# Performance work log

Hardware: AMD Instinct MI355X
Metric: run time of the kernel (lower is better)

Reference implementation:

```python
import jax, jax.numpy as jnp
import numpy as np

V, E, H = 32000, 512, 1024
B, T = 32, 48
PAD = 0


def setup_inputs() -> dict:
    key = jax.random.key(0)
    ks = jax.random.split(key, 9)
    s = 0.05
    emb = jax.random.normal(ks[0], (V, E), jnp.float32) * s
    emb = emb.at[PAD].set(0.0)  # padding_idx row is zero in nn.Embedding
    return {
        "initial_hidden_state": jax.random.normal(ks[1], (B, H), jnp.float32),
        "target_sequence": jax.random.randint(ks[2], (B, T), 0, V),
        "emb": emb,
        "W_ih": jax.random.normal(ks[3], (3 * H, E), jnp.float32) * s,  # [r;z;n] input weights
        "W_hh": jax.random.normal(ks[4], (3 * H, H), jnp.float32) * s,
        "b_ih": jax.random.normal(ks[5], (3 * H,), jnp.float32) * s,
        "b_hh": jax.random.normal(ks[6], (3 * H,), jnp.float32) * s,
        "W_cls": jax.random.normal(ks[7], (V, H), jnp.float32) * s,
        "b_cls": jax.random.normal(ks[8], (V,), jnp.float32) * s,
    }


def _decode(initial_hidden_state, target_sequence, emb, W_ih, W_hh, b_ih, b_hh, W_cls, b_cls):
    # teacher forcing: sample_probability = 0.0 -> use_sample False
    idx_t = target_sequence.T  # [T, B]

    def step(h, y_idx):
        x = emb[y_idx]                                 # [B, E] embedding gather
        gi = x @ W_ih.T + b_ih                         # [B, 3H]
        gh = h @ W_hh.T + b_hh                         # [B, 3H]
        i_r, i_z, i_n = jnp.split(gi, 3, axis=-1)
        h_r, h_z, h_n = jnp.split(gh, 3, axis=-1)
        r = jax.nn.sigmoid(i_r + h_r)
        z = jax.nn.sigmoid(i_z + h_z)
        n = jnp.tanh(i_n + r * h_n)
        h_new = (1.0 - z) * n + z * h                  # torch GRUCell update
        score = h_new @ W_cls.T + b_cls                # [B, V]
        return h_new, score

    _, scores = jax.lax.scan(step, initial_hidden_state, idx_t)  # [T, B, V]
    return jnp.transpose(scores, (1, 0, 2))                      # [B, T, V]


def reference(initial_hidden_state, target_sequence, emb, W_ih, W_hh, b_ih, b_hh, W_cls, b_cls):
    return _decode(initial_hidden_state, target_sequence, emb, W_ih, W_hh, b_ih, b_hh, W_cls, b_cls)
```

## Files before the change

### kernel.cpp

```cpp
#include <hip/hip_runtime.h>
#include <hip/hip_bf16.h>

typedef __attribute__((ext_vector_type(8))) short short8;
typedef __attribute__((ext_vector_type(4))) float f32x4;

#define T_STEPS 48
#define BATCH 32
#define EDIM 512
#define HDIM 1024
#define VOCAB 32000
#define GRU_BLOCKS 64
#define JPB 16
#define SENT 0x7FFF7FFFu
#define N_TILES 750
#define CNT_STRIDE 16
#define EARLY_WORKERS 128

#define HS_T_STRIDE 16384

__device__ __forceinline__ unsigned short f2bf(float f) {
    __hip_bfloat16 h = __float2bfloat16(f);
    return *reinterpret_cast<unsigned short*>(&h);
}
__device__ __forceinline__ float bf2f(unsigned short u) {
    union { unsigned int i; float f; } v;
    v.i = ((unsigned int)u) << 16;
    return v.f;
}

typedef __attribute__((address_space(1))) const void GAS;
typedef __attribute__((address_space(3))) void LAS;
__device__ __forceinline__ void gload_lds16(const unsigned short* g, unsigned short* l) {
    __builtin_amdgcn_global_load_lds((GAS*)g, (LAS*)(unsigned)(uintptr_t)l, 16, 0, 0);
}

__global__ __launch_bounds__(256) void prep_kernel(
    const float* __restrict__ h0, const int* __restrict__ tseq,
    const float* __restrict__ emb, const float* __restrict__ w_ih,
    const float* __restrict__ w_hh, const float* __restrict__ w_cls,
    unsigned short* __restrict__ wcls_bf, unsigned short* __restrict__ wih_bf,
    unsigned short* __restrict__ whh_bf, unsigned short* __restrict__ x_bf,
    unsigned int* __restrict__ hs32, unsigned int* __restrict__ cnt8)
{
    const long R0 = (long)VOCAB * HDIM / 4;
    const long R1 = (long)3 * HDIM * EDIM / 4;
    const long R2 = (long)3 * HDIM * HDIM / 4;
    const long R3 = (long)T_STEPS * BATCH * EDIM / 4;
    const long R4 = (long)HS_T_STRIDE;
    const long R5 = (long)T_STEPS * HS_T_STRIDE / 4;
    const long R6 = 512;
    const long total = R0 + R1 + R2 + R3 + R4 + R5 + R6;

    for (long i = (long)blockIdx.x * blockDim.x + threadIdx.x; i < total;
         i += (long)gridDim.x * blockDim.x) {
        if (i < R0) {
            float4 v = reinterpret_cast<const float4*>(w_cls)[i];
            ushort4 u = { f2bf(v.x), f2bf(v.y), f2bf(v.z), f2bf(v.w) };
            *reinterpret_cast<ushort4*>(wcls_bf + i * 4) = u;
        } else if (i < R0 + R1) {
            long j = i - R0;
            float4 v = reinterpret_cast<const float4*>(w_ih)[j];
            ushort4 u = { f2bf(v.x), f2bf(v.y), f2bf(v.z), f2bf(v.w) };
            *reinterpret_cast<ushort4*>(wih_bf + j * 4) = u;
        } else if (i < R0 + R1 + R2) {
            long j = i - R0 - R1;
            float4 v = reinterpret_cast<const float4*>(w_hh)[j];
            ushort4 u = { f2bf(v.x), f2bf(v.y), f2bf(v.z), f2bf(v.w) };
            *reinterpret_cast<ushort4*>(whh_bf + j * 4) = u;
        } else if (i < R0 + R1 + R2 + R3) {
            long j = i - R0 - R1 - R2;
            int m = (int)(j >> 7);
            int kk4 = (int)(j & 127);
            int t = m >> 5, b = m & 31;
            int tok = tseq[b * T_STEPS + t];
            float4 v = reinterpret_cast<const float4*>(emb)[(long)tok * (EDIM / 4) + kk4];
            ushort4 u = { f2bf(v.x), f2bf(v.y), f2bf(v.z), f2bf(v.w) };
            *reinterpret_cast<ushort4*>(x_bf + (long)m * EDIM + kk4 * 4) = u;
        } else if (i < R0 + R1 + R2 + R3 + R4) {
            long j = i - R0 - R1 - R2 - R3;
            int w = (int)(j >> 5), b = (int)(j & 31);
            unsigned short a = f2bf(h0[b * HDIM + 2 * w]);
            unsigned short c = f2bf(h0[b * HDIM + 2 * w + 1]);
            hs32[j] = (unsigned)a | ((unsigned)c << 16);
        } else if (i < R0 + R1 + R2 + R3 + R4 + R5) {
            long j = i - R0 - R1 - R2 - R3 - R4;
            uint4 s = { SENT, SENT, SENT, SENT };
            reinterpret_cast<uint4*>(hs32 + HS_T_STRIDE)[j] = s;
        } else {
            long j = i - R0 - R1 - R2 - R3 - R4 - R5;
            uint4 z = { 0u, 0u, 0u, 0u };
            reinterpret_cast<uint4*>(cnt8)[j] = z;
        }
    }
}

__global__ __launch_bounds__(256) void gemm_gi(
    const unsigned short* __restrict__ A, const unsigned short* __restrict__ B,
    const float* __restrict__ bias, float* __restrict__ C, int K, int Ntot, int nM)
{
    const int nwg = gridDim.x;
    const int lin = blockIdx.x;
    const int q = nwg >> 3;
    const int wg = (lin & 7) * q + (lin >> 3);
    const int mi = wg % nM, ni = wg / nM;
    const int m0 = mi * 128, n0 = ni * 128;

    const int tid = threadIdx.x;
    const int lane = tid & 63;
    const int wid = tid >> 6;
    const int wr = wid >> 1, wc = wid & 1;

    __shared__ __align__(16) unsigned short As[128 * 32];
    __shared__ __align__(16) unsigned short Bs[128 * 32];

    f32x4 acc[4][4] = {};
    const int NT = K >> 5;
    const int srow = (lane >> 2);
    const int skk = (lane & 3) * 8;

    for (int kt = 0; kt < NT; ++kt) {
        __syncthreads();
        {
            const int kb = kt * 32;
#pragma unroll
            for (int h2 = 0; h2 < 2; ++h2) {
                const int i = wid + h2 * 4;
                const int row = i * 16 + srow;
                gload_lds16(A + (size_t)(m0 + row) * K + kb + skk, As + i * 512);
                gload_lds16(B + (size_t)(n0 + row) * K + kb + skk, Bs + i * 512);
            }
        }
        __syncthreads();

        const int kg = lane >> 4;
        const int l15 = lane & 15;
        short8 af[4], bf[4];
#pragma unroll
        for (int i = 0; i < 4; ++i) {
            af[i] = *(const short8*)(As + ((wr * 64 + i * 16 + l15) * 32 + kg * 8));
            bf[i] = *(const short8*)(Bs + ((wc * 64 + i * 16 + l15) * 32 + kg * 8));
        }
#pragma unroll
        for (int i = 0; i < 4; ++i)
#pragma unroll
            for (int j = 0; j < 4; ++j)
                acc[i][j] = __builtin_amdgcn_mfma_f32_16x16x32_bf16(af[i], bf[j], acc[i][j], 0, 0, 0);
    }

    const int l15 = lane & 15, lhi = lane >> 4;
#pragma unroll
    for (int i = 0; i < 4; ++i)
#pragma unroll
        for (int j = 0; j < 4; ++j) {
            int col = n0 + wc * 64 + j * 16 + l15;
            float bv = bias[col];
#pragma unroll
            for (int q2 = 0; q2 < 4; ++q2) {
                int row = m0 + wr * 64 + i * 16 + lhi * 4 + q2;
                C[(size_t)row * Ntot + col] = acc[i][j][q2] + bv;
            }
        }
}

__global__ __launch_bounds__(512, 1) void fused_kernel(
    unsigned int* __restrict__ hs32, unsigned int* __restrict__ hrow32,
    const unsigned short* __restrict__ whh_bf,
    const float* __restrict__ gi, const float* __restrict__ b_hh,
    const float* __restrict__ h0,
    const unsigned short* __restrict__ wcls_bf, const float* __restrict__ b_cls,
    float* __restrict__ out, unsigned int* __restrict__ cnt8,
    unsigned int* __restrict__ tileq)
{
    __shared__ __align__(16) unsigned short Wl[48][1032];
    __shared__ float P[4][32][49];
    __shared__ __align__(16) unsigned short As[256 * 32];
    __shared__ __align__(16) unsigned short Bs[256 * 32];
    __shared__ int sTile;

    const int tid = threadIdx.x;
    const int bid = blockIdx.x;
    const int lane = tid & 63, wid = tid >> 6;
    const int l15 = lane & 15, kg = lane >> 4;

    if (bid < GRU_BLOCKS) {
        const int j0 = bid * JPB;
        for (int c = tid; c < 48 * 128; c += 512) {
            int row = c >> 7, k8 = (c & 127) * 8;
            int g = row >> 4, jj = row & 15;
            *(short8*)&Wl[row][k8] =
                *(const short8*)(whh_bf + (size_t)(g * HDIM + j0 + jj) * HDIM + k8);
        }
        const int b = tid >> 4, jj = tid & 15;
        const int gj = j0 + jj;
        const float bhr = b_hh[gj];
        const float bhz = b_hh[HDIM + gj];
        const float bhn = b_hh[2 * HDIM + gj];
        float hloc = h0[b * HDIM + gj];
        __syncthreads();

        for (int t = 0; t < T_STEPS; ++t) {
            const size_t tb = (size_t)t * HS_T_STRIDE;
            const float* gr = gi + (size_t)(t * BATCH + b) * (3 * HDIM);
            float xr = gr[gj], xz = gr[HDIM + gj], xn = gr[2 * HDIM + gj];

            if (t) {
                if (wid == 0) {
                    const unsigned int* cp = cnt8 + (size_t)t * CNT_STRIDE;
                    for (;;) {
                        unsigned v = (lane < 8)
                            ? __hip_atomic_load(cp + lane, __ATOMIC_RELAXED, __HIP_MEMORY_SCOPE_AGENT)
                            : 8u;
                        if (__all(v >= 8u)) break;
                        __builtin_amdgcn_s_sleep(2);
                    }
                }
                __syncthreads();
                asm volatile("" ::: "memory");
            }

            if (tid < 256) {
                const int kq = wid * 256;
                unsigned wv[8][8];
#pragma unroll
                for (int ks = 0; ks < 8; ++ks) {
                    const int wbase = wid * 128 + ks * 16 + kg * 4;
#pragma unroll
                    for (int mi2 = 0; mi2 < 2; ++mi2) {
                        const int bb = mi2 * 16 + l15;
#pragma unroll
                        for (int q = 0; q < 4; ++q)
                            wv[ks][mi2 * 4 + q] = *(const unsigned*)(
                                hs32 + tb + (size_t)(wbase + q) * 32 + bb);
                    }
                }
                for (;;) {
                    int bad = 0;
#pragma unroll
                    for (int ks = 0; ks < 8; ++ks)
#pragma unroll
                        for (int i = 0; i < 8; ++i)
                            bad |= (wv[ks][i] == SENT);
                    if (!__any(bad)) break;
                    __builtin_amdgcn_s_sleep(1);
#pragma unroll
                    for (int ks = 0; ks < 8; ++ks)
#pragma unroll
                        for (int i = 0; i < 8; ++i)
                            if (wv[ks][i] == SENT) {
                                const int mi2 = i >> 2, q = i & 3;
                                wv[ks][i] = __hip_atomic_load(
                                    hs32 + tb + (size_t)(wid * 128 + ks * 16 + kg * 4 + q) * 32 + (mi2 * 16 + l15),
                                    __ATOMIC_RELAXED, __HIP_MEMORY_SCOPE_AGENT);
                            }
                }
                f32x4 acc[2][3] = {};
#pragma unroll
                for (int ks = 0; ks < 8; ++ks) {
                    const int kb = kq + ks * 32 + kg * 8;
                    union U8 { unsigned u[4]; short8 s; };
                    short8 ah[2];
#pragma unroll
                    for (int mi2 = 0; mi2 < 2; ++mi2) {
                        U8 x;
#pragma unroll
                        for (int q = 0; q < 4; ++q) x.u[q] = wv[ks][mi2 * 4 + q];
                        ah[mi2] = x.s;
                    }
#pragma unroll
                    for (int fr = 0; fr < 3; ++fr) {
                        short8 bh = *(const short8*)&Wl[fr * 16 + l15][kb];
#pragma unroll
                        for (int mi2 = 0; mi2 < 2; ++mi2)
                            acc[mi2][fr] = __builtin_amdgcn_mfma_f32_16x16x32_bf16(ah[mi2], bh, acc[mi2][fr], 0, 0, 0);
                    }
                }
#pragma unroll
                for (int mi2 = 0; mi2 < 2; ++mi2)
#pragma unroll
                    for (int fr = 0; fr < 3; ++fr)
#pragma unroll
                        for (int q = 0; q < 4; ++q)
                            P[wid][mi2 * 16 + kg * 4 + q][fr * 16 + l15] = acc[mi2][fr][q];
            }
            __syncthreads();

            {
                float ghr = 0.f, ghz = 0.f, ghn = 0.f;
#pragma unroll
                for (int w = 0; w < 4; ++w) {
                    ghr += P[w][b][jj];
                    ghz += P[w][b][16 + jj];
                    ghn += P[w][b][32 + jj];
                }
                float r = 1.f / (1.f + __expf(-(xr + ghr + bhr)));
                float z = 1.f / (1.f + __expf(-(xz + ghz + bhz)));
                float n = tanhf(xn + r * (ghn + bhn));
                float hnew = (1.f - z) * n + z * hloc;
                hloc = hnew;
                unsigned hv = f2bf(hnew);
                unsigned nb = (unsigned)__shfl_xor((int)hv, 1);
                if (!(jj & 1)) {
                    unsigned w1 = hv | (nb << 16);
                    const int wdx = gj >> 1;
                    __hip_atomic_store(hs32 + (size_t)(t + 1) * HS_T_STRIDE + (size_t)wdx * 32 + b,
                                       w1, __ATOMIC_RELAXED, __HIP_MEMORY_SCOPE_AGENT);
                    __hip_atomic_store(hrow32 + ((size_t)t * BATCH + b) * 512 + wdx,
                                       w1, __ATOMIC_RELAXED, __HIP_MEMORY_SCOPE_AGENT);
                }
            }
            __syncthreads();
            if (tid == 0)
                __hip_atomic_fetch_add(cnt8 + (size_t)(t + 1) * CNT_STRIDE + (bid & 7), 1u,
                                       __ATOMIC_RELAXED, __HIP_MEMORY_SCOPE_AGENT);
        }
    } else if (bid >= GRU_BLOCKS + EARLY_WORKERS) {
        if (wid == 0) {
            const unsigned int* cp = cnt8 + (size_t)T_STEPS * CNT_STRIDE;
            for (;;) {
                unsigned v = (lane < 8)
                    ? __hip_atomic_load(cp + lane, __ATOMIC_RELAXED, __HIP_MEMORY_SCOPE_AGENT)
                    : 8u;
                if (__all(v >= 8u)) break;
                __builtin_amdgcn_s_sleep(64);
            }
        }
        __syncthreads();
    }

    const unsigned short* hrowA = (const unsigned short*)hrow32;
    const int srow = lane >> 2;
    const int skk = (lane & 3) * 8;
    const int wm = wid >> 1, wn = wid & 1;

    for (;;) {
        __syncthreads();
        if (tid == 0)
            sTile = (int)__hip_atomic_fetch_add(tileq, 1u, __ATOMIC_RELAXED, __HIP_MEMORY_SCOPE_AGENT);
        __syncthreads();
        const int k = sTile;
        if (k >= N_TILES) break;
        const int mi = k / 125, ni = k - mi * 125;
        const int m0 = mi * 256, n0 = ni * 256;

        {
            if (wid == 0) {
                const unsigned int* cp = cnt8 + (size_t)(mi * 8 + 8) * CNT_STRIDE;
                for (;;) {
                    unsigned v = (lane < 8)
                        ? __hip_atomic_load(cp + lane, __ATOMIC_RELAXED, __HIP_MEMORY_SCOPE_AGENT)
                        : 8u;
                    if (__all(v >= 8u)) break;
                    __builtin_amdgcn_s_sleep(32);
                }
            }
            __syncthreads();
            asm volatile("" ::: "memory");
        }

        f32x4 acc[4][8] = {};
        for (int kt = 0; kt < 32; ++kt) {
            __syncthreads();
            {
                const int kb = kt * 32;
#pragma unroll
                for (int h2 = 0; h2 < 2; ++h2) {
                    const int i = wid + h2 * 8;
                    const int row = i * 16 + srow;
                    gload_lds16(hrowA + (size_t)(m0 + row) * HDIM + kb + skk, As + i * 512);
                    gload_lds16(wcls_bf + (size_t)(n0 + row) * HDIM + kb + skk, Bs + i * 512);
                }
            }
            __syncthreads();

            short8 af[4], bf[8];
#pragma unroll
            for (int i = 0; i < 4; ++i)
                af[i] = *(const short8*)(As + ((wm * 64 + i * 16 + l15) * 32 + kg * 8));
#pragma unroll
            for (int j = 0; j < 8; ++j)
                bf[j] = *(const short8*)(Bs + ((wn * 128 + j * 16 + l15) * 32 + kg * 8));
#pragma unroll
            for (int i = 0; i < 4; ++i)
#pragma unroll
                for (int j = 0; j < 8; ++j)
                    acc[i][j] = __builtin_amdgcn_mfma_f32_16x16x32_bf16(af[i], bf[j], acc[i][j], 0, 0, 0);
        }

        const int lhi = lane >> 4;
#pragma unroll
        for (int i = 0; i < 4; ++i)
#pragma unroll
            for (int j = 0; j < 8; ++j) {
                int col = n0 + wn * 128 + j * 16 + l15;
                float bv = b_cls[col];
#pragma unroll
                for (int q2 = 0; q2 < 4; ++q2) {
                    int row = m0 + wm * 64 + i * 16 + lhi * 4 + q2;
                    int t = row >> 5, bb = row & 31;
                    __builtin_nontemporal_store(acc[i][j][q2] + bv,
                        &out[(size_t)(bb * T_STEPS + t) * VOCAB + col]);
                }
            }
    }
}

extern "C" void kernel_launch(void* const* d_in, const int* in_sizes, int n_in,
                              void* d_out, int out_size, void* d_ws, size_t ws_size,
                              hipStream_t stream) {
    const float* h0    = (const float*)d_in[0];
    const int*   tseq  = (const int*)d_in[1];
    const float* emb   = (const float*)d_in[2];
    const float* w_ih  = (const float*)d_in[3];
    const float* w_hh  = (const float*)d_in[4];
    const float* b_ih  = (const float*)d_in[5];
    const float* b_hh  = (const float*)d_in[6];
    const float* w_cls = (const float*)d_in[7];
    const float* b_cls = (const float*)d_in[8];
    float* out = (float*)d_out;

    char* w = (char*)d_ws;
    unsigned short* wcls_bf = (unsigned short*)w; w += (size_t)VOCAB * HDIM * 2;
    unsigned short* wih_bf  = (unsigned short*)w; w += (size_t)3 * HDIM * EDIM * 2;
    unsigned short* whh_bf  = (unsigned short*)w; w += (size_t)3 * HDIM * HDIM * 2;
    unsigned short* x_bf    = (unsigned short*)w; w += (size_t)T_STEPS * BATCH * EDIM * 2;
    unsigned int*   hs32    = (unsigned int*)w;   w += (size_t)(T_STEPS + 1) * HS_T_STRIDE * 4;
    unsigned int*   hrow32  = (unsigned int*)w;   w += (size_t)T_STEPS * BATCH * 512 * 4;
    float* gi               = (float*)w;          w += (size_t)T_STEPS * BATCH * 3 * HDIM * 4;
    unsigned int* cnt8      = (unsigned int*)w;   w += 8192;
    unsigned int* tileq     = cnt8 + 1024;

    prep_kernel<<<2048, 256, 0, stream>>>(h0, tseq, emb, w_ih, w_hh, w_cls,
                                          wcls_bf, wih_bf, whh_bf, x_bf, hs32, cnt8);

    gemm_gi<<<(T_STEPS * BATCH / 128) * (3 * HDIM / 128), 256, 0, stream>>>(
        x_bf, wih_bf, b_ih, gi, EDIM, 3 * HDIM, T_STEPS * BATCH / 128);

    fused_kernel<<<256, 512, 0, stream>>>(hs32, hrow32, whh_bf, gi, b_hh, h0,
                                          wcls_bf, b_cls, out, cnt8, tileq);
}
```

Before: 384.0 us.

## Double-buffer classifier GEMM LDS tiles and vectorize hidden-state publication

The classifier GEMM loop now uses two LDS buffers so that the global-to-LDS load for the next K slice is issued while MFMAs run on the current one, removing one barrier per K step. Shared memory is unioned between the GRU weight cache and the GEMM buffers to make room for this. The GRU blocks also stage new hidden values in LDS and publish them with 16-byte coherent (sc0 sc1) stores instead of many scalar atomic stores. The risk is that the second buffer's loads may not be waited for correctly, and that the recurrence path gains an extra barrier per step.

```diff
diff --git a/kernel.cpp b/kernel.cpp
--- a/kernel.cpp
+++ b/kernel.cpp
@@ -3,6 +3,7 @@
 
 typedef __attribute__((ext_vector_type(8))) short short8;
 typedef __attribute__((ext_vector_type(4))) float f32x4;
+typedef __attribute__((ext_vector_type(4))) unsigned int u32x4;
 
 #define T_STEPS 48
 #define BATCH 32
@@ -32,6 +33,11 @@
 typedef __attribute__((address_space(3))) void LAS;
 __device__ __forceinline__ void gload_lds16(const unsigned short* g, unsigned short* l) {
     __builtin_amdgcn_global_load_lds((GAS*)g, (LAS*)(unsigned)(uintptr_t)l, 16, 0, 0);
+}
+
+__device__ __forceinline__ void store16_coh(unsigned int* p, u32x4 v) {
+    asm volatile("global_store_dwordx4 %0, %1, off sc0 sc1"
+                 :: "v"((unsigned long long)(uintptr_t)p), "v"(v) : "memory");
 }
 
 __global__ __launch_bounds__(256) void prep_kernel(
@@ -171,10 +177,8 @@
     float* __restrict__ out, unsigned int* __restrict__ cnt8,
     unsigned int* __restrict__ tileq)
 {
-    __shared__ __align__(16) unsigned short Wl[48][1032];
-    __shared__ float P[4][32][49];
-    __shared__ __align__(16) unsigned short As[256 * 32];
-    __shared__ __align__(16) unsigned short Bs[256 * 32];
+    __shared__ __align__(16) char smem[124160];
+    __shared__ unsigned short Hs[BATCH][JPB];
     __shared__ int sTile;
 
     const int tid = threadIdx.x;
@@ -183,6 +187,9 @@
     const int l15 = lane & 15, kg = lane >> 4;
 
     if (bid < GRU_BLOCKS) {
+        unsigned short (*Wl)[1032] = reinterpret_cast<unsigned short (*)[1032]>(smem);
+        float (*P)[32][49] = reinterpret_cast<float (*)[32][49]>(smem + 99072);
+
         const int j0 = bid * JPB;
         for (int c = tid; c < 48 * 128; c += 512) {
             int row = c >> 7, k8 = (c & 127) * 8;
@@ -297,16 +304,28 @@
                 float n = tanhf(xn + r * (ghn + bhn));
                 float hnew = (1.f - z) * n + z * hloc;
                 hloc = hnew;
-                unsigned hv = f2bf(hnew);
-                unsigned nb = (unsigned)__shfl_xor((int)hv, 1);
-                if (!(jj & 1)) {
-                    unsigned w1 = hv | (nb << 16);
-                    const int wdx = gj >> 1;
-                    __hip_atomic_store(hs32 + (size_t)(t + 1) * HS_T_STRIDE + (size_t)wdx * 32 + b,
-                                       w1, __ATOMIC_RELAXED, __HIP_MEMORY_SCOPE_AGENT);
-                    __hip_atomic_store(hrow32 + ((size_t)t * BATCH + b) * 512 + wdx,
-                                       w1, __ATOMIC_RELAXED, __HIP_MEMORY_SCOPE_AGENT);
-                }
+                Hs[b][jj] = f2bf(hnew);
+            }
+            __syncthreads();
+
+            if (tid < 64) {
+                const int q = tid >> 3, c = tid & 7;
+                u32x4 d;
+#pragma unroll
+                for (int w2 = 0; w2 < 4; ++w2) {
+                    int bb = c * 4 + w2;
+                    d[w2] = (unsigned)Hs[bb][2 * q] | ((unsigned)Hs[bb][2 * q + 1] << 16);
+                }
+                store16_coh(hs32 + (size_t)(t + 1) * HS_T_STRIDE + (size_t)((j0 >> 1) + q) * 32 + c * 4, d);
+            } else if (tid < 128) {
+                const int i = tid - 64, bb = i >> 1, half = i & 1;
+                u32x4 d;
+#pragma unroll
+                for (int w2 = 0; w2 < 4; ++w2) {
+                    int q = half * 4 + w2;
+                    d[w2] = (unsigned)Hs[bb][2 * q] | ((unsigned)Hs[bb][2 * q + 1] << 16);
+                }
+                store16_coh(hrow32 + ((size_t)t * BATCH + bb) * 512 + (j0 >> 1) + half * 4, d);
             }
             __syncthreads();
             if (tid == 0)
@@ -332,6 +351,11 @@
     const int skk = (lane & 3) * 8;
     const int wm = wid >> 1, wn = wid & 1;
 
+    unsigned short* As0 = (unsigned short*)(smem);
+    unsigned short* Bs0 = (unsigned short*)(smem + 16384);
+    unsigned short* As1 = (unsigned short*)(smem + 32768);
+    unsigned short* Bs1 = (unsigned short*)(smem + 49152);
+
     for (;;) {
         __syncthreads();
         if (tid == 0)
@@ -358,33 +382,47 @@
         }
 
         f32x4 acc[4][8] = {};
-        for (int kt = 0; kt < 32; ++kt) {
-            __syncthreads();
-            {
-                const int kb = kt * 32;
-#pragma unroll
-                for (int h2 = 0; h2 < 2; ++h2) {
-                    const int i = wid + h2 * 8;
-                    const int row = i * 16 + srow;
-                    gload_lds16(hrowA + (size_t)(m0 + row) * HDIM + kb + skk, As + i * 512);
-                    gload_lds16(wcls_bf + (size_t)(n0 + row) * HDIM + kb + skk, Bs + i * 512);
-                }
-            }
-            __syncthreads();
-
-            short8 af[4], bf[8];
-#pragma unroll
-            for (int i = 0; i < 4; ++i)
-                af[i] = *(const short8*)(As + ((wm * 64 + i * 16 + l15) * 32 + kg * 8));
-#pragma unroll
-            for (int j = 0; j < 8; ++j)
-                bf[j] = *(const short8*)(Bs + ((wn * 128 + j * 16 + l15) * 32 + kg * 8));
-#pragma unroll
-            for (int i = 0; i < 4; ++i)
-#pragma unroll
-                for (int j = 0; j < 8; ++j)
-                    acc[i][j] = __builtin_amdgcn_mfma_f32_16x16x32_bf16(af[i], bf[j], acc[i][j], 0, 0, 0);
-        }
+
+#define STAGE(KT, AB, BB)                                                      \
+        {                                                                      \
+            const int kb = (KT) * 32;                                          \
+            _Pragma("unroll")                                                  \
+            for (int h2 = 0; h2 < 2; ++h2) {                                   \
+                const int i = wid + h2 * 8;                                    \
+                const int row = i * 16 + srow;                                 \
+                gload_lds16(hrowA + (size_t)(m0 + row) * HDIM + kb + skk, (AB) + i * 512); \
+                gload_lds16(wcls_bf + (size_t)(n0 + row) * HDIM + kb + skk, (BB) + i * 512); \
+            }                                                                  \
+        }
+#define COMPUTE(AB, BB)                                                        \
+        {                                                                      \
+            short8 af[4], bf[8];                                               \
+            _Pragma("unroll")                                                  \
+            for (int i = 0; i < 4; ++i)                                        \
+                af[i] = *(const short8*)((AB) + ((wm * 64 + i * 16 + l15) * 32 + kg * 8)); \
+            _Pragma("unroll")                                                  \
+            for (int j = 0; j < 8; ++j)                                        \
+                bf[j] = *(const short8*)((BB) + ((wn * 128 + j * 16 + l15) * 32 + kg * 8)); \
+            _Pragma("unroll")                                                  \
+            for (int i = 0; i < 4; ++i)                                        \
+                _Pragma("unroll")                                              \
+                for (int j = 0; j < 8; ++j)                                    \
+                    acc[i][j] = __builtin_amdgcn_mfma_f32_16x16x32_bf16(af[i], bf[j], acc[i][j], 0, 0, 0); \
+        }
+
+        STAGE(0, As0, Bs0);
+        __syncthreads();
+        for (int it = 0; it < 16; ++it) {
+            const int kt0 = 2 * it;
+            STAGE(kt0 + 1, As1, Bs1);
+            COMPUTE(As0, Bs0);
+            __syncthreads();
+            if (kt0 + 2 < 32) STAGE(kt0 + 2, As0, Bs0);
+            COMPUTE(As1, Bs1);
+            __syncthreads();
+        }
+#undef STAGE
+#undef COMPUTE
 
         const int lhi = lane >> 4;
 #pragma unroll
```

Result: faster. 345.4 us (-10.1%).
